# Kernel tuning notes

Measured on AMD Instinct MI355X. Metric: run time of the kernel, lower is better.

## Reference

```python
import jax, jax.numpy as jnp
import numpy as np


def _conv3x3(x, w, b):
    # stride 1, padding 1, NCHW / OIHW
    y = jax.lax.conv_general_dilated(x, w, (1, 1), ((1, 1), (1, 1)),
                                     dimension_numbers=('NCHW', 'OIHW', 'NCHW'))
    return y + b[None, :, None, None]


def _bilinear(img, py, px):
    """Bilinear sample img [B,C,H,W] at float positions py,px [B,H,W].
    Out-of-bounds corners contribute zero (zero padding), matching DCNv2."""
    B, C, H, W = img.shape
    y0f = jnp.floor(py)
    x0f = jnp.floor(px)
    wy = (py - y0f)[:, None]  # [B,1,H,W]
    wx = (px - x0f)[:, None]
    y0 = y0f.astype(jnp.int32)
    x0 = x0f.astype(jnp.int32)
    flat = img.reshape(B, C, H * W)

    def g(iy, ix):
        valid = ((iy >= 0) & (iy < H) & (ix >= 0) & (ix < W))
        lin = (jnp.clip(iy, 0, H - 1) * W + jnp.clip(ix, 0, W - 1)).reshape(B, 1, -1)
        idx = jnp.broadcast_to(lin, (B, C, lin.shape[-1]))
        v = jnp.take_along_axis(flat, idx, axis=2).reshape(B, C, *iy.shape[1:])
        return v * valid[:, None].astype(img.dtype)

    v00 = g(y0, x0)
    v01 = g(y0, x0 + 1)
    v10 = g(y0 + 1, x0)
    v11 = g(y0 + 1, x0 + 1)
    return (v00 * (1 - wy) * (1 - wx) + v01 * (1 - wy) * wx
            + v10 * wy * (1 - wx) + v11 * wy * wx)


def _dcn(x, ow, ob, w, b):
    """Modulated deformable conv (DCNv2), 3x3, stride 1, pad 1, dg=1."""
    B, C, H, W = x.shape
    om = _conv3x3(x, ow, ob)                       # [B,27,H,W]
    o1, o2, m = jnp.split(om, 3, axis=1)
    off = jnp.concatenate([o1, o2], axis=1)        # [B,18,H,W]
    mask = jax.nn.sigmoid(m)                       # [B,9,H,W]
    oy = off[:, 0::2]                              # [B,9,H,W] y-offset per tap
    ox = off[:, 1::2]                              # [B,9,H,W] x-offset per tap
    ys = jnp.arange(H, dtype=x.dtype)[None, :, None]
    xs = jnp.arange(W, dtype=x.dtype)[None, None, :]
    acc = jnp.zeros((B, w.shape[0], H, W), x.dtype)
    for k in range(9):  # fixed small kernel-tap loop
        ky, kx = divmod(k, 3)
        py = ys + (ky - 1) + oy[:, k]
        px = xs + (kx - 1) + ox[:, k]
        v = _bilinear(x, py, px) * mask[:, k][:, None]   # [B,C,H,W]
        acc = acc + jnp.einsum('bchw,oc->bohw', v, w[:, :, ky, kx])
    return acc + b[None, :, None, None]


def setup_inputs() -> dict:
    key = jax.random.key(0)
    ks = jax.random.split(key, 8)
    B, H, W = 4, 96, 96
    x = jax.random.normal(ks[0], (B, 64, H, W), jnp.float32)

    def offw(k, cin):
        return jax.random.normal(k, (27, cin, 3, 3), jnp.float32) * 0.01

    def mainw(k, cout, cin):
        return jax.random.normal(k, (cout, cin, 3, 3), jnp.float32) * (1.0 / np.sqrt(cin * 9))

    return {
        'x': x,
        'ow1': offw(ks[1], 64), 'ob1': jnp.zeros((27,), jnp.float32),
        'w1': mainw(ks[2], 64, 64), 'b1': jnp.zeros((64,), jnp.float32),
        'ow2': offw(ks[3], 64), 'ob2': jnp.zeros((27,), jnp.float32),
        'w2': mainw(ks[4], 512, 64), 'b2': jnp.zeros((512,), jnp.float32),
        'ow3': offw(ks[5], 512), 'ob3': jnp.zeros((27,), jnp.float32),
        'w3': mainw(ks[6], 256, 512), 'b3': jnp.zeros((256,), jnp.float32),
    }


def reference(x, ow1, ob1, w1, b1, ow2, ob2, w2, b2, ow3, ob3, w3, b3):
    y = _dcn(x, ow1, ob1, w1, b1)
    y = _dcn(y, ow2, ob2, w2, b2)
    y = _dcn(y, ow3, ob3, w3, b3)
    return y
```

## Files before the change

kernel.cpp:

```cpp
#include <hip/hip_runtime.h>
#include <stdint.h>


#define HH 96
#define WW 96
#define BBATCH 4
#define HWP (HH*WW)
#define PTOT (BBATCH*HWP)

typedef _Float16 f16x8 __attribute__((ext_vector_type(8)));
typedef _Float16 h2    __attribute__((ext_vector_type(2)));
typedef float f32x4 __attribute__((ext_vector_type(4)));

union U16x8 { uint4 q; _Float16 h[8]; h2 v[4]; };
union UB    { uint4 q; f16x8 f; };
union UH4   { uint2 d; _Float16 h[4]; };

__global__ void k_nchw2nhwc(const float* __restrict__ in, _Float16* __restrict__ out){
  __shared__ float t[32][33];
  int b = blockIdx.z;
  int p0 = blockIdx.x*32, c0 = blockIdx.y*32;
  int tx = threadIdx.x, ty = threadIdx.y;
  #pragma unroll
  for(int i=0;i<32;i+=8)
    t[ty+i][tx] = in[((size_t)(b*64 + c0+ty+i))*HWP + p0+tx];
  __syncthreads();
  #pragma unroll
  for(int i=0;i<32;i+=8)
    out[((size_t)(b*HWP + p0+ty+i))*64 + c0+tx] = (_Float16)t[tx][ty+i];
}

template<int CIN>
__global__ void k_tow(const float* __restrict__ ow, _Float16* __restrict__ owT){
  int i = blockIdx.x*256 + threadIdx.x;
  if(i >= 9*32*CIN) return;
  int c = i % CIN; int j = (i/CIN)&31; int k = i/(CIN*32);
  owT[i] = (j<27) ? (_Float16)ow[((size_t)(j*CIN + c))*9 + k] : (_Float16)0.f;
}

template<int CIN,int COUT>
__global__ void k_tw(const float* __restrict__ w, _Float16* __restrict__ wTf){
  int i = blockIdx.x*256 + threadIdx.x;
  if(i >= 9*COUT*CIN) return;
  int c = i % CIN; int o = (i/CIN)%COUT; int k = i/(CIN*COUT);
  int g = c>>5, quad = (c>>3)&3, j = c&7;
  int ob = o>>4, l15 = o&15;
  size_t dst = ((((size_t)k*(CIN/32) + g)*(COUT/16) + ob)*64 + quad*16 + l15)*8 + j;
  wTf[dst] = (_Float16)w[((size_t)(o*CIN + c))*9 + k];
}

template<int CIN,int NT>
__launch_bounds__(256,2)
__global__ void k_goffs(const _Float16* __restrict__ xin, const _Float16* __restrict__ owT,
                        float* __restrict__ om){
  int t = threadIdx.x;
  int lane = t&63, wave = t>>6;
  int quad = lane>>4, l15 = lane&15;
  f32x4 acc[2] = {};
  int pos0, K0;
  float* omo;

  if constexpr (CIN >= 128){
    constexpr int NZ = (NT==3) ? 3 : 1;
    int bx = blockIdx.x;
    int q = bx>>3, r = bx&7;
    int z = q - (q/NZ)*NZ;
    int lin = r*((gridDim.x>>3)/NZ) + q/NZ;
    pos0 = lin*64;
    K0 = z*NT;
    omo = om + (size_t)z*PTOT*32;

    constexpr int SPT = CIN/64;
    constexpr int S = NT*SPT;
    __shared__ __align__(16) _Float16 As[2][64*72];
    __shared__ __align__(16) _Float16 Bs[2][32*72];
    int pa = t>>2, ca = (t&3)*16;
    int jb = t>>3, cb = (t&7)*8;
    int P = pos0 + pa;
    int b = P/HWP, rem = P%HWP;
    int y = rem/WW, x = rem%WW;
    const _Float16* baseA = xin + (size_t)b*HWP*CIN + ca;
    const uint4 zz = make_uint4(0,0,0,0);
    int ofsC, ofsN = 0; bool vldC, vldN = false; int ktC, ktN = 0;
    {
      int iy = y + K0/3 - 1, ix = x + K0%3 - 1;
      vldC = (iy>=0)&&(iy<HH)&&(ix>=0)&&(ix<WW);
      int cy = min(max(iy,0),HH-1), cx = min(max(ix,0),WW-1);
      ofsC = (cy*WW+cx)*CIN; ktC = K0;
    }
    {
      uint4 a0 = vldC ? *(const uint4*)(baseA + ofsC)     : zz;
      uint4 a1 = vldC ? *(const uint4*)(baseA + ofsC + 8) : zz;
      uint4 bv = *(const uint4*)(owT + ((size_t)ktC*32 + jb)*CIN + cb);
      *(uint4*)&As[0][pa*72 + ca]     = a0;
      *(uint4*)&As[0][pa*72 + ca + 8] = a1;
      *(uint4*)&Bs[0][jb*72 + cb]     = bv;
    }
    uint4 nA0 = vldC ? *(const uint4*)(baseA + ofsC + 64)     : zz;
    uint4 nA1 = vldC ? *(const uint4*)(baseA + ofsC + 64 + 8) : zz;
    uint4 nAb = *(const uint4*)(owT + ((size_t)ktC*32 + jb)*CIN + 64 + cb);
    uint4 nB0, nB1, nBb;
    int buf = 0;

    #pragma unroll 1
    for(int ss=0; ss<S; ss+=2){
      {
        const int s = ss;
        __syncthreads();
        if(s > 0 && (s % SPT) == 0){ ofsC=ofsN; vldC=vldN; ktC=ktN; }
        if(s+2 < S){
          int sm2 = (s+2) % SPT;
          if(sm2 == 0){
            int k = K0 + (s+2)/SPT;
            int iy = y + k/3 - 1, ix = x + k%3 - 1;
            vldN = (iy>=0)&&(iy<HH)&&(ix>=0)&&(ix<WW);
            int cy = min(max(iy,0),HH-1), cx = min(max(ix,0),WW-1);
            ofsN = (cy*WW+cx)*CIN; ktN = k;
          }
          bool useN = (sm2 < 2);
          int ofs = useN ? ofsN : ofsC;
          bool vld = useN ? vldN : vldC;
          int kt  = useN ? ktN  : ktC;
          int c0 = sm2*64;
          nB0 = vld ? *(const uint4*)(baseA + ofs + c0)     : zz;
          nB1 = vld ? *(const uint4*)(baseA + ofs + c0 + 8) : zz;
          nBb = *(const uint4*)(owT + ((size_t)kt*32 + jb)*CIN + c0 + cb);
        }
        UB afu0, afu1;
        afu0.q = *(const uint4*)&As[buf][(wave*16 + l15)*72 + quad*8];
        afu1.q = *(const uint4*)&As[buf][(wave*16 + l15)*72 + 32 + quad*8];
        #pragma unroll
        for(int ni=0;ni<2;ni++){
          UB bu0, bu1;
          bu0.q = *(const uint4*)&Bs[buf][(ni*16 + l15)*72 + quad*8];
          bu1.q = *(const uint4*)&Bs[buf][(ni*16 + l15)*72 + 32 + quad*8];
          acc[ni] = __builtin_amdgcn_mfma_f32_16x16x32_f16(afu0.f, bu0.f, acc[ni], 0,0,0);
          acc[ni] = __builtin_amdgcn_mfma_f32_16x16x32_f16(afu1.f, bu1.f, acc[ni], 0,0,0);
        }
        if(s+1 < S){
          *(uint4*)&As[buf^1][pa*72 + ca]     = nA0;
          *(uint4*)&As[buf^1][pa*72 + ca + 8] = nA1;
          *(uint4*)&Bs[buf^1][jb*72 + cb]     = nAb;
        }
        buf ^= 1;
      }
      {
        const int s = ss+1;
        __syncthreads();
        if((s % SPT) == 0){ ofsC=ofsN; vldC=vldN; ktC=ktN; }
        if(s+2 < S){
          int sm2 = (s+2) % SPT;
          if(sm2 == 0){
            int k = K0 + (s+2)/SPT;
            int iy = y + k/3 - 1, ix = x + k%3 - 1;
            vldN = (iy>=0)&&(iy<HH)&&(ix>=0)&&(ix<WW);
            int cy = min(max(iy,0),HH-1), cx = min(max(ix,0),WW-1);
            ofsN = (cy*WW+cx)*CIN; ktN = k;
          }
          bool useN = (sm2 < 2);
          int ofs = useN ? ofsN : ofsC;
          bool vld = useN ? vldN : vldC;
          int kt  = useN ? ktN  : ktC;
          int c0 = sm2*64;
          nA0 = vld ? *(const uint4*)(baseA + ofs + c0)     : zz;
          nA1 = vld ? *(const uint4*)(baseA + ofs + c0 + 8) : zz;
          nAb = *(const uint4*)(owT + ((size_t)kt*32 + jb)*CIN + c0 + cb);
        }
        UB afu0, afu1;
        afu0.q = *(const uint4*)&As[buf][(wave*16 + l15)*72 + quad*8];
        afu1.q = *(const uint4*)&As[buf][(wave*16 + l15)*72 + 32 + quad*8];
        #pragma unroll
        for(int ni=0;ni<2;ni++){
          UB bu0, bu1;
          bu0.q = *(const uint4*)&Bs[buf][(ni*16 + l15)*72 + quad*8];
          bu1.q = *(const uint4*)&Bs[buf][(ni*16 + l15)*72 + 32 + quad*8];
          acc[ni] = __builtin_amdgcn_mfma_f32_16x16x32_f16(afu0.f, bu0.f, acc[ni], 0,0,0);
          acc[ni] = __builtin_amdgcn_mfma_f32_16x16x32_f16(afu1.f, bu1.f, acc[ni], 0,0,0);
        }
        if(s+1 < S){
          *(uint4*)&As[buf^1][pa*72 + ca]     = nB0;
          *(uint4*)&As[buf^1][pa*72 + ca + 8] = nB1;
          *(uint4*)&Bs[buf^1][jb*72 + cb]     = nBb;
        }
        buf ^= 1;
      }
    }
  } else {
    pos0 = blockIdx.x*64;
    K0 = blockIdx.y*NT;
    omo = om + (size_t)blockIdx.y*PTOT*32;
    __shared__ __align__(16) _Float16 As[64*40];
    __shared__ __align__(16) _Float16 Bs[32*40];
    int pa = t>>2, ca = (t&3)*8;
    int P = pos0 + pa;
    int b = P/HWP, rem = P%HWP;
    int y = rem/WW, x = rem%WW;
    #pragma unroll 1
    for(int k=K0;k<K0+NT;k++){
      int iy = y + k/3 - 1, ix = x + k%3 - 1;
      bool valid = (iy>=0)&&(iy<HH)&&(ix>=0)&&(ix<WW);
      const _Float16* src = xin + (((size_t)b*HWP + iy*WW + ix)*CIN) + ca;
      #pragma unroll 1
      for(int c0=0;c0<CIN;c0+=32){
        uint4 av = make_uint4(0,0,0,0);
        if(valid) av = *(const uint4*)(src + c0);
        *(uint4*)&As[pa*40 + ca] = av;
        if(t < 128){
          int j = t>>2;
          *(uint4*)&Bs[j*40 + ca] = *(const uint4*)(owT + ((size_t)k*32 + j)*CIN + c0 + ca);
        }
        __syncthreads();
        UB afu; afu.q = *(const uint4*)&As[(wave*16 + l15)*40 + quad*8];
        #pragma unroll
        for(int ni=0;ni<2;ni++){
          UB bu; bu.q = *(const uint4*)&Bs[(ni*16 + l15)*40 + quad*8];
          acc[ni] = __builtin_amdgcn_mfma_f32_16x16x32_f16(afu.f, bu.f, acc[ni], 0,0,0);
        }
        __syncthreads();
      }
    }
  }

  #pragma unroll
  for(int ni=0;ni<2;ni++)
    #pragma unroll
    for(int r=0;r<4;r++){
      int row = wave*16 + quad*4 + r;
      omo[(size_t)(pos0+row)*32 + ni*16 + l15] = acc[ni][r];
    }
}

template<int NS>
__global__ void k_prep(const float* __restrict__ om, const float* __restrict__ ob,
                       float* __restrict__ pym){
  int i = blockIdx.x*256 + threadIdx.x;
  if(i >= PTOT*9) return;
  int k = i%9, p = i/9;
  int rem = p%HWP;
  int y = rem/WW, x = rem%WW;
  float oy=0.f, ox=0.f, mm=0.f;
  #pragma unroll
  for(int s=0;s<NS;s++){
    const float* o = om + (size_t)s*PTOT*32 + (size_t)p*32;
    oy += o[2*k]; ox += o[2*k+1]; mm += o[18+k];
  }
  oy += ob[2*k]; ox += ob[2*k+1]; mm += ob[18+k];
  float m = 1.f/(1.f + expf(-mm));
  pym[(size_t)i*3+0] = (float)(y + k/3 - 1) + oy;
  pym[(size_t)i*3+1] = (float)(x + k%3 - 1) + ox;
  pym[(size_t)i*3+2] = m;
}

template<int CIN,int COUT,int BN,int MODE>
__launch_bounds__(256,2)
__global__ void k_gmain(const _Float16* __restrict__ xin, const float* __restrict__ pym,
                        const _Float16* __restrict__ wTf, const float* __restrict__ bias,
                        void* __restrict__ outv){
  constexpr int NW = BN/4;
  constexpr int NF = NW/16;
  constexpr int KG = CIN/32;
  constexpr int OB = COUT/16;
  constexpr int SPT = CIN/64;
  constexpr int NZ = (MODE==1) ? 3 : 1;
  constexpr int KN = (MODE==1) ? 3 : 9;
  constexpr int S = KN*SPT;
  __shared__ __align__(16) _Float16 As[2][64*72];
  int bx = blockIdx.x;
  int q = bx>>3, r = bx&7;
  int z = q - (q/NZ)*NZ;
  int lin = r*((gridDim.x>>3)/NZ) + q/NZ;
  int pos0 = lin*64;
  int o0 = blockIdx.y*BN;
  int K0 = (MODE==1) ? z*3 : 0;
  int t = threadIdx.x;
  int lane = t&63, wave = t>>6;
  int quad = lane>>4, l15 = lane&15;
  f32x4 acc[4][NF] = {};
  int pa = t>>2, ca = (t&3)*16;
  int P = pos0 + pa;
  int b = P/HWP;
  const _Float16* base = xin + (size_t)b*HWP*CIN + ca;
  const uint4* wf = (const uint4*)wTf;
  int obBase = (o0>>4) + wave*NF;

  auto tapParams = [&](int k, h2* W, int* oc){
    const float* pp = pym + ((size_t)P*9 + k)*3;
    float py = pp[0], px = pp[1], mk = pp[2];
    float y0f = floorf(py), x0f = floorf(px);
    float wy = py - y0f, wx = px - x0f;
    int iy0 = (int)y0f, ix0 = (int)x0f;
    int iy1 = iy0+1, ix1 = ix0+1;
    bool vy0 = (iy0>=0)&&(iy0<HH), vy1 = (iy1>=0)&&(iy1<HH);
    bool vx0 = (ix0>=0)&&(ix0<WW), vx1 = (ix1>=0)&&(ix1<WW);
    float w00 = (vy0&&vx0) ? (1.f-wy)*(1.f-wx)*mk : 0.f;
    float w01 = (vy0&&vx1) ? (1.f-wy)*wx*mk      : 0.f;
    float w10 = (vy1&&vx0) ? wy*(1.f-wx)*mk      : 0.f;
    float w11 = (vy1&&vx1) ? wy*wx*mk            : 0.f;
    int cy0 = min(max(iy0,0),HH-1), cy1 = min(max(iy1,0),HH-1);
    int cx0 = min(max(ix0,0),WW-1), cx1 = min(max(ix1,0),WW-1);
    W[0] = h2{(_Float16)w00,(_Float16)w00};
    W[1] = h2{(_Float16)w01,(_Float16)w01};
    W[2] = h2{(_Float16)w10,(_Float16)w10};
    W[3] = h2{(_Float16)w11,(_Float16)w11};
    oc[0] = (cy0*WW+cx0)*CIN;
    oc[1] = (cy0*WW+cx1)*CIN;
    oc[2] = (cy1*WW+cx0)*CIN;
    oc[3] = (cy1*WW+cx1)*CIN;
  };

  uint4 Bq[2][NF];
  const uint4* wB = wf + (size_t)(K0*KG)*OB*64 + lane;
  int buf = 0;

  if constexpr (SPT > 1){
    h2 Wcur[4], Wnxt[4];
    int ocCur[4], ocNxt[4];
    tapParams(K0, Wcur, ocCur);
    U16x8 ncA[4][2], ncB[4][2];
    {
      U16x8 c0v[4][2];
      #pragma unroll
      for(int c=0;c<4;c++){
        const _Float16* pp = base + ocCur[c];
        c0v[c][0].q = *(const uint4*)(pp);
        c0v[c][1].q = *(const uint4*)(pp + 8);
      }
      #pragma unroll
      for(int ks=0;ks<2;ks++)
        #pragma unroll
        for(int ni=0;ni<NF;ni++)
          Bq[ks][ni] = wB[(size_t)ks*OB*64 + (size_t)(obBase+ni)*64];
      wB += 2*OB*64;
      U16x8 rr0, rr1;
      #pragma unroll
      for(int j=0;j<4;j++){
        rr0.v[j] = c0v[0][0].v[j]*Wcur[0] + c0v[1][0].v[j]*Wcur[1] + c0v[2][0].v[j]*Wcur[2] + c0v[3][0].v[j]*Wcur[3];
        rr1.v[j] = c0v[0][1].v[j]*Wcur[0] + c0v[1][1].v[j]*Wcur[1] + c0v[2][1].v[j]*Wcur[2] + c0v[3][1].v[j]*Wcur[3];
      }
      *(uint4*)&As[0][pa*72 + ca]     = rr0.q;
      *(uint4*)&As[0][pa*72 + ca + 8] = rr1.q;
      #pragma unroll
      for(int c=0;c<4;c++){
        const _Float16* pp = base + ocCur[c] + 64;
        ncA[c][0].q = *(const uint4*)(pp);
        ncA[c][1].q = *(const uint4*)(pp + 8);
      }
    }

    auto stage = [&](int s, U16x8 (&ncC)[4][2], U16x8 (&ncN)[4][2]){
      __syncthreads();
      bool more  = (s+1 < S);
      bool more2 = (s+2 < S);
      if(s > 0 && (s % SPT) == 0){
        #pragma unroll
        for(int j=0;j<4;j++){ Wcur[j]=Wnxt[j]; ocCur[j]=ocNxt[j]; }
      }
      if(more2){
        int sm2 = (s+2) % SPT;
        if(sm2 == 0) tapParams(K0 + (s+2)/SPT, Wnxt, ocNxt);
        bool useNxt = (sm2 < 2);
        int ocS[4];
        #pragma unroll
        for(int c=0;c<4;c++) ocS[c] = useNxt ? ocNxt[c] : ocCur[c];
        int c0 = sm2*64;
        #pragma unroll
        for(int c=0;c<4;c++){
          const _Float16* pp = base + ocS[c] + c0;
          ncN[c][0].q = *(const uint4*)(pp);
          ncN[c][1].q = *(const uint4*)(pp + 8);
        }
      }
      UB afu[2][4];
      #pragma unroll
      for(int ks=0;ks<2;ks++)
        #pragma unroll
        for(int mi=0;mi<4;mi++)
          afu[ks][mi].q = *(const uint4*)&As[buf][(mi*16 + l15)*72 + ks*32 + quad*8];
      #pragma unroll
      for(int ks=0;ks<2;ks++)
        #pragma unroll
        for(int ni=0;ni<NF;ni++){
          UB bu; bu.q = Bq[ks][ni];
          #pragma unroll
          for(int mi=0;mi<4;mi++)
            acc[mi][ni] = __builtin_amdgcn_mfma_f32_16x16x32_f16(afu[ks][mi].f, bu.f, acc[mi][ni], 0,0,0);
        }
      if(more){
        #pragma unroll
        for(int ks=0;ks<2;ks++)
          #pragma unroll
          for(int ni=0;ni<NF;ni++)
            Bq[ks][ni] = wB[(size_t)ks*OB*64 + (size_t)(obBase+ni)*64];
        wB += 2*OB*64;
        bool lerpNxt = (((s+1) % SPT) == 0);
        h2 Wl[4];
        #pragma unroll
        for(int j=0;j<4;j++) Wl[j] = lerpNxt ? Wnxt[j] : Wcur[j];
        U16x8 rr0, rr1;
        #pragma unroll
        for(int j=0;j<4;j++){
          rr0.v[j] = ncC[0][0].v[j]*Wl[0] + ncC[1][0].v[j]*Wl[1] + ncC[2][0].v[j]*Wl[2] + ncC[3][0].v[j]*Wl[3];
          rr1.v[j] = ncC[0][1].v[j]*Wl[0] + ncC[1][1].v[j]*Wl[1] + ncC[2][1].v[j]*Wl[2] + ncC[3][1].v[j]*Wl[3];
        }
        *(uint4*)&As[buf^1][pa*72 + ca]     = rr0.q;
        *(uint4*)&As[buf^1][pa*72 + ca + 8] = rr1.q;
      }
      buf ^= 1;
    };

    #pragma unroll 1
    for(int ss=0; ss<S; ss+=2){
      stage(ss,   ncA, ncB);
      stage(ss+1, ncB, ncA);
    }
  } else {
    h2 Wc[4]; int oc_[4];
    h2 Wn[4]; int ocn[4];
    tapParams(K0, Wc, oc_);
    {
      U16x8 nc[4][2];
      #pragma unroll
      for(int c=0;c<4;c++){
        const _Float16* pp = base + oc_[c];
        nc[c][0].q = *(const uint4*)(pp);
        nc[c][1].q = *(const uint4*)(pp + 8);
      }
      #pragma unroll
      for(int ks=0;ks<2;ks++)
        #pragma unroll
        for(int ni=0;ni<NF;ni++)
          Bq[ks][ni] = wB[(size_t)ks*OB*64 + (size_t)(obBase+ni)*64];
      wB += 2*OB*64;
      U16x8 rr0, rr1;
      #pragma unroll
      for(int j=0;j<4;j++){
        rr0.v[j] = nc[0][0].v[j]*Wc[0] + nc[1][0].v[j]*Wc[1] + nc[2][0].v[j]*Wc[2] + nc[3][0].v[j]*Wc[3];
        rr1.v[j] = nc[0][1].v[j]*Wc[0] + nc[1][1].v[j]*Wc[1] + nc[2][1].v[j]*Wc[2] + nc[3][1].v[j]*Wc[3];
      }
      *(uint4*)&As[0][pa*72 + ca]     = rr0.q;
      *(uint4*)&As[0][pa*72 + ca + 8] = rr1.q;
    }
    if(S>1) tapParams(K0+1, Wn, ocn);

    #pragma unroll 1
    for(int s=0;s<S;s++){
      __syncthreads();
      U16x8 nc[4][2];
      bool more = (s+1 < S);
      if(more){
        #pragma unroll
        for(int c=0;c<4;c++){ Wc[c]=Wn[c]; oc_[c]=ocn[c]; }
        #pragma unroll
        for(int c=0;c<4;c++){
          const _Float16* pp = base + oc_[c];
          nc[c][0].q = *(const uint4*)(pp);
          nc[c][1].q = *(const uint4*)(pp + 8);
        }
      }
      UB afu[2][4];
      #pragma unroll
      for(int ks=0;ks<2;ks++)
        #pragma unroll
        for(int mi=0;mi<4;mi++)
          afu[ks][mi].q = *(const uint4*)&As[buf][(mi*16 + l15)*72 + ks*32 + quad*8];
      #pragma unroll
      for(int ks=0;ks<2;ks++)
        #pragma unroll
        for(int ni=0;ni<NF;ni++){
          UB bu; bu.q = Bq[ks][ni];
          #pragma unroll
          for(int mi=0;mi<4;mi++)
            acc[mi][ni] = __builtin_amdgcn_mfma_f32_16x16x32_f16(afu[ks][mi].f, bu.f, acc[mi][ni], 0,0,0);
        }
      if(more){
        #pragma unroll
        for(int ks=0;ks<2;ks++)
          #pragma unroll
          for(int ni=0;ni<NF;ni++)
            Bq[ks][ni] = wB[(size_t)ks*OB*64 + (size_t)(obBase+ni)*64];
        wB += 2*OB*64;
        if(s+2 < S) tapParams(K0+s+2, Wn, ocn);
        U16x8 rr0, rr1;
        #pragma unroll
        for(int j=0;j<4;j++){
          rr0.v[j] = nc[0][0].v[j]*Wc[0] + nc[1][0].v[j]*Wc[1] + nc[2][0].v[j]*Wc[2] + nc[3][0].v[j]*Wc[3];
          rr1.v[j] = nc[0][1].v[j]*Wc[0] + nc[1][1].v[j]*Wc[1] + nc[2][1].v[j]*Wc[2] + nc[3][1].v[j]*Wc[3];
        }
        *(uint4*)&As[buf^1][pa*72 + ca]     = rr0.q;
        *(uint4*)&As[buf^1][pa*72 + ca + 8] = rr1.q;
      }
      buf ^= 1;
    }
  }

  #pragma unroll
  for(int mi=0;mi<4;mi++){
    #pragma unroll
    for(int ni=0;ni<NF;ni++){
      int col = o0 + wave*NW + ni*16 + l15;
      if(MODE==1){
        float* out = (float*)outv + (size_t)z*PTOT*COUT;
        #pragma unroll
        for(int r=0;r<4;r++){
          int row = pos0 + mi*16 + quad*4 + r;
          out[(size_t)row*COUT + col] = acc[mi][ni][r];
        }
      } else {
        float bo = bias[col];
        _Float16* out = (_Float16*)outv;
        #pragma unroll
        for(int r=0;r<4;r++){
          int row = pos0 + mi*16 + quad*4 + r;
          out[(size_t)row*COUT + col] = (_Float16)(acc[mi][ni][r]+bo);
        }
      }
    }
  }
}

template<int COUT>
__global__ void k_redA(const float* __restrict__ part, const float* __restrict__ bias,
                       _Float16* __restrict__ out){
  int i4 = blockIdx.x*256 + threadIdx.x;
  constexpr int N4 = PTOT*COUT/4;
  if(i4 >= N4) return;
  const float4* p = (const float4*)part;
  float4 a = p[i4], b = p[i4 + N4], c = p[i4 + 2*N4];
  int col0 = (i4*4) & (COUT-1);
  float4 bi = *(const float4*)(bias + col0);
  UH4 r;
  r.h[0] = (_Float16)(a.x+b.x+c.x+bi.x);
  r.h[1] = (_Float16)(a.y+b.y+c.y+bi.y);
  r.h[2] = (_Float16)(a.z+b.z+c.z+bi.z);
  r.h[3] = (_Float16)(a.w+b.w+c.w+bi.w);
  *(uint2*)(out + (size_t)i4*4) = r.d;
}

__global__ void k_redT(const float* __restrict__ part, const float* __restrict__ bias,
                       float* __restrict__ out){
  __shared__ float t[32][33];
  constexpr int COUT = 256;
  constexpr size_t SL = (size_t)PTOT*COUT;
  int b = blockIdx.z;
  int p0 = blockIdx.x*32, c0 = blockIdx.y*32;
  int tx = threadIdx.x, ty = threadIdx.y;
  #pragma unroll
  for(int i=0;i<32;i+=8){
    size_t idx = ((size_t)(b*HWP + p0+ty+i))*COUT + c0+tx;
    t[ty+i][tx] = part[idx] + part[idx+SL] + part[idx+2*SL];
  }
  __syncthreads();
  #pragma unroll
  for(int i=0;i<32;i+=8)
    out[((size_t)(b*COUT + c0+ty+i))*HWP + p0+tx] = t[tx][ty+i] + bias[c0+ty+i];
}

extern "C" void kernel_launch(void* const* d_in, const int* in_sizes, int n_in,
                              void* d_out, int out_size, void* d_ws, size_t ws_size,
                              hipStream_t stream){
  (void)in_sizes; (void)n_in; (void)out_size;
  const float* x   = (const float*)d_in[0];
  const float* ow1 = (const float*)d_in[1];
  const float* ob1 = (const float*)d_in[2];
  const float* w1  = (const float*)d_in[3];
  const float* b1  = (const float*)d_in[4];
  const float* ow2 = (const float*)d_in[5];
  const float* ob2 = (const float*)d_in[6];
  const float* w2  = (const float*)d_in[7];
  const float* b2  = (const float*)d_in[8];
  const float* ow3 = (const float*)d_in[9];
  const float* ob3 = (const float*)d_in[10];
  const float* w3  = (const float*)d_in[11];
  const float* b3  = (const float*)d_in[12];

  char* p = (char*)d_ws;
  auto carve = [&](size_t bytes)->char*{ char* r = p; p += (bytes + 255) & ~(size_t)255; return r; };
  _Float16* xh  = (_Float16*)carve((size_t)PTOT*64*2);
  _Float16* y1  = (_Float16*)carve((size_t)PTOT*64*2);
  _Float16* y2  = (_Float16*)carve((size_t)PTOT*512*2);
  _Float16* owT = (_Float16*)carve((size_t)9*32*512*2);
  _Float16* wT  = (_Float16*)carve((size_t)9*512*512*2);
  float*    om  = (float*)carve((size_t)3*PTOT*32*4);
  float*    pym = (float*)carve((size_t)PTOT*9*3*4);
  bool splitK = ws_size >= ((size_t)p - (size_t)d_ws) + (size_t)3*PTOT*256*4 + 4096;
  float* part = splitK ? (float*)carve((size_t)3*PTOT*256*4) : nullptr;

  k_nchw2nhwc<<<dim3(288,2,BBATCH), dim3(32,8), 0, stream>>>(x, xh);

  if(splitK){
    k_tow<64><<<(9*32*64+255)/256,256,0,stream>>>(ow1, owT);
    k_tw<64,64><<<(9*64*64+255)/256,256,0,stream>>>(w1, wT);
    k_goffs<64,3><<<dim3(PTOT/64,3),256,0,stream>>>(xh, owT, om);
    k_prep<3><<<(PTOT*9+255)/256,256,0,stream>>>(om, ob1, pym);
    k_gmain<64,64,64,1><<<dim3(3*PTOT/64,1,1),256,0,stream>>>(xh, pym, wT, b1, part);
    k_redA<64><<<(PTOT*64/4+255)/256,256,0,stream>>>(part, b1, y1);

    k_tow<64><<<(9*32*64+255)/256,256,0,stream>>>(ow2, owT);
    k_tw<64,512><<<(9*512*64+255)/256,256,0,stream>>>(w2, wT);
    k_goffs<64,3><<<dim3(PTOT/64,3),256,0,stream>>>(y1, owT, om);
    k_prep<3><<<(PTOT*9+255)/256,256,0,stream>>>(om, ob2, pym);
    k_gmain<64,512,256,0><<<dim3(PTOT/64,2),256,0,stream>>>(y1, pym, wT, b2, y2);

    k_tow<512><<<(9*32*512+255)/256,256,0,stream>>>(ow3, owT);
    k_tw<512,256><<<(9*256*512+255)/256,256,0,stream>>>(w3, wT);
    k_goffs<512,3><<<dim3(3*PTOT/64,1),256,0,stream>>>(y2, owT, om);
    k_prep<3><<<(PTOT*9+255)/256,256,0,stream>>>(om, ob3, pym);
    k_gmain<512,256,256,1><<<dim3(3*PTOT/64,1,1),256,0,stream>>>(y2, pym, wT, b3, part);
    k_redT<<<dim3(288,8,4),dim3(32,8),0,stream>>>(part, b3, (float*)d_out);
  } else {
    k_tow<64><<<(9*32*64+255)/256,256,0,stream>>>(ow1, owT);
    k_tw<64,64><<<(9*64*64+255)/256,256,0,stream>>>(w1, wT);
    k_goffs<64,9><<<dim3(PTOT/64,1),256,0,stream>>>(xh, owT, om);
    k_prep<1><<<(PTOT*9+255)/256,256,0,stream>>>(om, ob1, pym);
    k_gmain<64,64,64,0><<<dim3(PTOT/64,1),256,0,stream>>>(xh, pym, wT, b1, y1);

    k_tow<64><<<(9*32*64+255)/256,256,0,stream>>>(ow2, owT);
    k_tw<64,512><<<(9*512*64+255)/256,256,0,stream>>>(w2, wT);
    k_goffs<64,9><<<dim3(PTOT/64,1),256,0,stream>>>(y1, owT, om);
    k_prep<1><<<(PTOT*9+255)/256,256,0,stream>>>(om, ob2, pym);
    k_gmain<64,512,256,0><<<dim3(PTOT/64,2),256,0,stream>>>(y1, pym, wT, b2, y2);

    k_tow<512><<<(9*32*512+255)/256,256,0,stream>>>(ow3, owT);
    k_tw<512,256><<<(9*256*512+255)/256,256,0,stream>>>(w3, wT);
    k_goffs<512,9><<<dim3(PTOT/64,1),256,0,stream>>>(y2, owT, om);
    k_prep<1><<<(PTOT*9+255)/256,256,0,stream>>>(om, ob3, pym);
    k_gmain<512,256,256,0><<<dim3(PTOT/64,1),256,0,stream>>>(y2, pym, wT, b3, y1);
    {
      struct L { static __global__ void tr(const _Float16* in, float* out){
        int i = blockIdx.x*256 + threadIdx.x;
        if(i >= PTOT*256) return;
        int c = i & 255, pnt = i >> 8;
        int bb = pnt / HWP, pr = pnt % HWP;
        out[((size_t)bb*256 + c)*HWP + pr] = (float)in[i];
      }};
      hipLaunchKernelGGL(L::tr, dim3((PTOT*256+255)/256), dim3(256), 0, stream,
                         (const _Float16*)y1, (float*)d_out);
    }
  }
}
```

Before: 381.5 us.

## Run layer-3 deformable GEMM with 512-thread blocks and eight waves

Adds a THREADS template parameter to the main deformable GEMM kernel and a 512-thread path for the large-CIN case. Each block now uses eight waves, so each wave owns fewer output columns (smaller NF). Each thread gathers 8 channels instead of 16 per bilinear corner, with a simpler single-buffer prefetch of the next stage. The aim is more latency hiding and lower per-thread register pressure for the layer-3 GEMM. The cost is more threads contending per block at the same launch-bounds occupancy target, and less work per thread to amortise barriers.

```diff
diff --git a/kernel.cpp b/kernel.cpp
--- a/kernel.cpp
+++ b/kernel.cpp
@@ -251,12 +251,13 @@
   pym[(size_t)i*3+2] = m;
 }
 
-template<int CIN,int COUT,int BN,int MODE>
-__launch_bounds__(256,2)
+template<int CIN,int COUT,int BN,int MODE,int THREADS=256>
+__launch_bounds__(THREADS,2)
 __global__ void k_gmain(const _Float16* __restrict__ xin, const float* __restrict__ pym,
                         const _Float16* __restrict__ wTf, const float* __restrict__ bias,
                         void* __restrict__ outv){
-  constexpr int NW = BN/4;
+  constexpr int WAVES = THREADS/64;
+  constexpr int NW = BN/WAVES;
   constexpr int NF = NW/16;
   constexpr int KG = CIN/32;
   constexpr int OB = COUT/16;
@@ -264,6 +265,8 @@
   constexpr int NZ = (MODE==1) ? 3 : 1;
   constexpr int KN = (MODE==1) ? 3 : 9;
   constexpr int S = KN*SPT;
+  constexpr int TPR = THREADS/64;
+  constexpr int CPT = 64/TPR;
   __shared__ __align__(16) _Float16 As[2][64*72];
   int bx = blockIdx.x;
   int q = bx>>3, r = bx&7;
@@ -276,7 +279,7 @@
   int lane = t&63, wave = t>>6;
   int quad = lane>>4, l15 = lane&15;
   f32x4 acc[4][NF] = {};
-  int pa = t>>2, ca = (t&3)*16;
+  int pa = t/TPR, ca = (t%TPR)*CPT;
   int P = pos0 + pa;
   int b = P/HWP;
   const _Float16* base = xin + (size_t)b*HWP*CIN + ca;
@@ -312,7 +315,68 @@
   const uint4* wB = wf + (size_t)(K0*KG)*OB*64 + lane;
   int buf = 0;
 
-  if constexpr (SPT > 1){
+  if constexpr (SPT > 1 && THREADS == 512){
+    h2 Wc[4]; int oc_[4];
+    tapParams(K0, Wc, oc_);
+    {
+      U16x8 nc[4];
+      #pragma unroll
+      for(int c=0;c<4;c++) nc[c].q = *(const uint4*)(base + oc_[c]);
+      #pragma unroll
+      for(int ks=0;ks<2;ks++)
+        #pragma unroll
+        for(int ni=0;ni<NF;ni++)
+          Bq[ks][ni] = wB[(size_t)ks*OB*64 + (size_t)(obBase+ni)*64];
+      wB += 2*OB*64;
+      U16x8 rr;
+      #pragma unroll
+      for(int j=0;j<4;j++)
+        rr.v[j] = nc[0].v[j]*Wc[0] + nc[1].v[j]*Wc[1] + nc[2].v[j]*Wc[2] + nc[3].v[j]*Wc[3];
+      *(uint4*)&As[0][pa*72 + ca] = rr.q;
+    }
+    #pragma unroll 1
+    for(int s=0;s<S;s++){
+      __syncthreads();
+      U16x8 nc[4];
+      bool more = (s+1 < S);
+      if(more){
+        int sn = s+1;
+        if((sn % SPT) == 0) tapParams(K0 + sn/SPT, Wc, oc_);
+        int c0 = (sn % SPT)*64;
+        #pragma unroll
+        for(int c=0;c<4;c++) nc[c].q = *(const uint4*)(base + oc_[c] + c0);
+      }
+      UB afu[2][4];
+      #pragma unroll
+      for(int ks=0;ks<2;ks++)
+        #pragma unroll
+        for(int mi=0;mi<4;mi++)
+          afu[ks][mi].q = *(const uint4*)&As[buf][(mi*16 + l15)*72 + ks*32 + quad*8];
+      #pragma unroll
+      for(int ks=0;ks<2;ks++)
+        #pragma unroll
+        for(int ni=0;ni<NF;ni++){
+          UB bu; bu.q = Bq[ks][ni];
+          #pragma unroll
+          for(int mi=0;mi<4;mi++)
+            acc[mi][ni] = __builtin_amdgcn_mfma_f32_16x16x32_f16(afu[ks][mi].f, bu.f, acc[mi][ni], 0,0,0);
+        }
+      if(more){
+        #pragma unroll
+        for(int ks=0;ks<2;ks++)
+          #pragma unroll
+          for(int ni=0;ni<NF;ni++)
+            Bq[ks][ni] = wB[(size_t)ks*OB*64 + (size_t)(obBase+ni)*64];
+        wB += 2*OB*64;
+        U16x8 rr;
+        #pragma unroll
+        for(int j=0;j<4;j++)
+          rr.v[j] = nc[0].v[j]*Wc[0] + nc[1].v[j]*Wc[1] + nc[2].v[j]*Wc[2] + nc[3].v[j]*Wc[3];
+        *(uint4*)&As[buf^1][pa*72 + ca] = rr.q;
+      }
+      buf ^= 1;
+    }
+  } else if constexpr (SPT > 1){
     h2 Wcur[4], Wnxt[4];
     int ocCur[4], ocNxt[4];
     tapParams(K0, Wcur, ocCur);
@@ -605,7 +669,7 @@
     k_tw<512,256><<<(9*256*512+255)/256,256,0,stream>>>(w3, wT);
     k_goffs<512,3><<<dim3(3*PTOT/64,1),256,0,stream>>>(y2, owT, om);
     k_prep<3><<<(PTOT*9+255)/256,256,0,stream>>>(om, ob3, pym);
-    k_gmain<512,256,256,1><<<dim3(3*PTOT/64,1,1),256,0,stream>>>(y2, pym, wT, b3, part);
+    k_gmain<512,256,256,1,512><<<dim3(3*PTOT/64,1,1),512,0,stream>>>(y2, pym, wT, b3, part);
     k_redT<<<dim3(288,8,4),dim3(32,8),0,stream>>>(part, b3, (float*)d_out);
   } else {
     k_tow<64><<<(9*32*64+255)/256,256,0,stream>>>(ow1, owT);
```

Result: no change. 384.9 us (+0.9%).
